# Kernel tuning notes

Measured on AMD Instinct MI355X. Metric: run time of the kernel, lower is better.

The kernel has to match this reference:

```python
import jax, jax.numpy as jnp
import numpy as np

N_HEAD = 16
HEAD_DIM = 64  # n_embd // n_head = 1024 // 16


def setup_inputs() -> dict:
    key = jax.random.key(0)
    k1, k2, k3 = jax.random.split(key, 3)
    B, T, C = 4, 2048, 1024
    x = jax.random.normal(k1, (B, T, C), dtype=jnp.float32)
    # torch Linear weight is (out, in); we store transposed (in, out) for x @ W
    w_qkv = jax.random.normal(k2, (C, 3 * C), dtype=jnp.float32) * (1.0 / np.sqrt(C))
    w_out = jax.random.normal(k3, (C, C), dtype=jnp.float32) * (1.0 / np.sqrt(C))
    return {"x": x, "w_qkv": w_qkv, "w_out": w_out}


def reference(x, w_qkv, w_out):
    B, T, C = x.shape
    scale = 1.0 / np.sqrt(HEAD_DIM).astype(np.float32)
    qkv = x @ w_qkv                                   # [B, T, 3C]
    q, k, v = jnp.split(qkv, 3, axis=2)
    def heads(t):  # [B, T, C] -> [B, H, T, Dh]
        return t.reshape(B, T, N_HEAD, HEAD_DIM).transpose(0, 2, 1, 3)
    q, k, v = heads(q), heads(k), heads(v)
    att = jnp.einsum('bhqd,bhkd->bhqk', q, k) * scale  # [B, H, T, T]
    causal = jnp.tril(jnp.ones((T, T), dtype=bool))
    att = jnp.where(causal[None, None], att, jnp.float32(-jnp.inf))
    att = jax.nn.softmax(att, axis=-1)
    y = jnp.einsum('bhqk,bhkd->bhqd', att, v)          # [B, H, T, Dh]
    y = y.transpose(0, 2, 1, 3).reshape(B, T, C)
    return y @ w_out
```

## Files before the change

kernel.cpp:

```cpp
#include <hip/hip_runtime.h>
#include <hip/hip_bf16.h>

#define B_ 4
#define T_ 2048
#define C_ 1024
#define H_ 16
#define D_ 64

typedef __bf16 bf16x8 __attribute__((ext_vector_type(8)));
typedef float f32x4 __attribute__((ext_vector_type(4)));
typedef float f32x16 __attribute__((ext_vector_type(16)));

__device__ __forceinline__ unsigned short f2bs(float f) {
    __hip_bfloat16 h = __float2bfloat16(f);
    return *reinterpret_cast<unsigned short*>(&h);
}

__device__ __forceinline__ float fexp2(float x) {
    float r;
    asm("v_exp_f32 %0, %1" : "=v"(r) : "v"(x));
    return r;
}

__device__ __forceinline__ unsigned cvtpk(float a, float b) {
    unsigned r;
    asm("v_cvt_pk_bf16_f32 %0, %1, %2" : "=v"(r) : "v"(a), "v"(b));
    return r;
}

__device__ __forceinline__ void plane32swap(unsigned& a, unsigned& b, int hi) {
#if __has_builtin(__builtin_amdgcn_permlane32_swap)
    typedef int i32x2 __attribute__((ext_vector_type(2)));
    i32x2 r = __builtin_amdgcn_permlane32_swap((int)a, (int)b, false, false);
    a = (unsigned)r.x; b = (unsigned)r.y;
#else
    unsigned v = hi ? a : b;
    unsigned e = __shfl_xor(v, 32);
    unsigned na = hi ? e : a;
    unsigned nb = hi ? b : e;
    a = na; b = nb;
#endif
}

__device__ __forceinline__ int swz(int row, int col) {
    return (row * 64 + col) ^ ((row & 7) << 3);
}

__device__ __forceinline__ void gload16(const void* g, void* l) {
    auto gp = (const __attribute__((address_space(1))) void*)(g);
    auto lp = (__attribute__((address_space(3))) void*)(uintptr_t)(l);
    __builtin_amdgcn_global_load_lds(gp, lp, 16, 0, 0);
}

__global__ __launch_bounds__(256)
void prep_fused(const float* __restrict__ x, unsigned short* __restrict__ xb,
                const float* __restrict__ in1, unsigned short* __restrict__ out1,
                const float* __restrict__ in2, unsigned short* __restrict__ out2) {
    __shared__ float tile[64][65];
    const int bid = blockIdx.x;
    if (bid < 8192) {
        int i = bid * 256 + threadIdx.x;
        float4 v = ((const float4*)x)[i];
        union { unsigned short h[4]; uint2 u; } pk;
        pk.h[0] = f2bs(v.x); pk.h[1] = f2bs(v.y);
        pk.h[2] = f2bs(v.z); pk.h[3] = f2bs(v.w);
        ((uint2*)xb)[i] = pk.u;
        return;
    }
    const int tb = bid - 8192;
    const int bx = tb & 63;
    const int by = tb >> 6;
    const int tx = threadIdx.x & 63;
    const int ty = threadIdx.x >> 6;
    const bool second = bx >= 48;
    const float* in = second ? in2 : in1;
    unsigned short* out = second ? out2 : out1;
    const int C = second ? 1024 : 3072;
    const int R = 1024;
    const int c0 = (second ? (bx - 48) : bx) * 64;
    const int r0 = by * 64;
    #pragma unroll
    for (int i = 0; i < 16; ++i) {
        int r = ty * 16 + i;
        tile[r][tx] = in[(size_t)(r0 + r) * C + c0 + tx];
    }
    __syncthreads();
    #pragma unroll
    for (int i = 0; i < 16; ++i) {
        int r = ty * 16 + i;
        out[(size_t)(c0 + r) * R + r0 + tx] = f2bs(tile[tx][r]);
    }
}

template<int MODE, int K>
__global__ __launch_bounds__(256, 5)
void gemm_bt32(const unsigned short* __restrict__ A,
               const unsigned short* __restrict__ Bt,
               float* __restrict__ Out, int N_out,
               unsigned short* __restrict__ Qb,
               unsigned short* __restrict__ Kb,
               unsigned short* __restrict__ Vt) {
    __shared__ alignas(16) unsigned short As[2][128 * 32];
    __shared__ alignas(16) unsigned short Bs[2][128 * 32];
    const int tid = threadIdx.x;
    const int l = tid & 63;
    const int c16 = l & 15, lq = l >> 4;
    const int wv = tid >> 6;
    const int wrow = wv >> 1, wcol = wv & 1;
    const int m0 = blockIdx.x * 128, n0 = blockIdx.y * 128;

    f32x4 acc[4][4];
    #pragma unroll
    for (int i = 0; i < 4; ++i)
        #pragma unroll
        for (int j = 0; j < 4; ++j)
            acc[i][j] = f32x4{0.f, 0.f, 0.f, 0.f};

    const int srow = tid >> 2;
    const int scs  = tid & 3;
    const int ldsbase = (tid & ~63) * 8;

    auto stage = [&](int k0, int buf) {
        #pragma unroll
        for (int p = 0; p < 2; ++p) {
            int row = p * 64 + srow;
            int csw = 8 * (scs ^ ((row >> 1) & 3));
            gload16(&A[(size_t)(m0 + row) * K + k0 + csw], &As[buf][p * 2048 + ldsbase]);
            gload16(&Bt[(size_t)(n0 + row) * K + k0 + csw], &Bs[buf][p * 2048 + ldsbase]);
        }
    };

    stage(0, 0);
    constexpr int NK = K >> 5;
    for (int i = 0; i < NK; ++i) {
        __syncthreads();
        if (i + 1 < NK) stage((i + 1) << 5, (i + 1) & 1);
        const unsigned short* Al = As[i & 1];
        const unsigned short* Bl = Bs[i & 1];
        bf16x8 af[4], bfv[4];
        #pragma unroll
        for (int t = 0; t < 4; ++t) {
            int arow = wrow * 64 + t * 16 + c16;
            int brow = wcol * 64 + t * 16 + c16;
            af[t]  = *(const bf16x8*)&Al[arow * 32 + ((lq ^ ((arow >> 1) & 3)) * 8)];
            bfv[t] = *(const bf16x8*)&Bl[brow * 32 + ((lq ^ ((brow >> 1) & 3)) * 8)];
        }
        #pragma unroll
        for (int mi = 0; mi < 4; ++mi)
            #pragma unroll
            for (int ni = 0; ni < 4; ++ni)
                acc[mi][ni] = __builtin_amdgcn_mfma_f32_16x16x32_bf16(
                    af[mi], bfv[ni], acc[mi][ni], 0, 0, 0);
    }

    #pragma unroll
    for (int mi = 0; mi < 4; ++mi) {
        #pragma unroll
        for (int ni = 0; ni < 4; ++ni) {
            #pragma unroll
            for (int r = 0; r < 4; ++r) {
                float v = acc[mi][ni][r];
                int row = m0 + wrow * 64 + mi * 16 + lq * 4 + r;
                int col = n0 + wcol * 64 + ni * 16 + c16;
                if (MODE == 1) {
                    Out[(size_t)row * N_out + col] = v;
                } else {
                    int which = col >> 10;
                    int c = col & 1023;
                    int h = c >> 6, d = c & 63;
                    int b = row >> 11, t = row & 2047;
                    int bh = b * H_ + h;
                    if (which == 0)
                        Qb[((size_t)(bh * T_ + t)) * D_ + d] = f2bs(v * 0.1803368801111204f);
                    else if (which == 1)
                        Kb[((size_t)(bh * T_ + t)) * D_ + d] = f2bs(v);
                    else
                        Vt[((size_t)(bh * D_ + d)) * T_ + t] = f2bs(v);
                }
            }
        }
    }
}

template<int MODE>
__global__ __launch_bounds__(256)
void gemm_bt(const unsigned short* __restrict__ A,
             const unsigned short* __restrict__ Bt,
             float* __restrict__ Out, int N_out,
             unsigned short* __restrict__ Qb,
             unsigned short* __restrict__ Kb,
             unsigned short* __restrict__ Vt,
             int K) {
    __shared__ alignas(16) unsigned short As[2][128 * 64];
    __shared__ alignas(16) unsigned short Bs[2][128 * 64];
    const int tid = threadIdx.x;
    const int l = tid & 63;
    const int c16 = l & 15, lq = l >> 4;
    const int wv = tid >> 6;
    const int wrow = wv >> 1, wcol = wv & 1;
    const int m0 = blockIdx.x * 128, n0 = blockIdx.y * 128;

    f32x4 acc[4][4];
    #pragma unroll
    for (int i = 0; i < 4; ++i)
        #pragma unroll
        for (int j = 0; j < 4; ++j)
            acc[i][j] = f32x4{0.f, 0.f, 0.f, 0.f};

    const int srow = tid >> 3;
    const int scs  = tid & 7;
    const int ldsbase = (tid & ~63) * 8;

    auto stage = [&](int k0, int buf) {
        #pragma unroll
        for (int p = 0; p < 4; ++p) {
            int row = p * 32 + srow;
            int csw = 8 * (scs ^ (row & 7));
            gload16(&A[(size_t)(m0 + row) * K + k0 + csw], &As[buf][p * 2048 + ldsbase]);
            gload16(&Bt[(size_t)(n0 + row) * K + k0 + csw], &Bs[buf][p * 2048 + ldsbase]);
        }
    };

    stage(0, 0);
    const int NK = K >> 6;
    for (int i = 0; i < NK; ++i) {
        __syncthreads();
        if (i + 1 < NK) stage((i + 1) << 6, (i + 1) & 1);
        const unsigned short* Al = As[i & 1];
        const unsigned short* Bl = Bs[i & 1];
        #pragma unroll
        for (int kk = 0; kk < 64; kk += 32) {
            bf16x8 af[4], bfv[4];
            int koff = kk + lq * 8;
            #pragma unroll
            for (int t = 0; t < 4; ++t) {
                af[t]  = *(const bf16x8*)&Al[swz(wrow * 64 + t * 16 + c16, koff)];
                bfv[t] = *(const bf16x8*)&Bl[swz(wcol * 64 + t * 16 + c16, koff)];
            }
            #pragma unroll
            for (int mi = 0; mi < 4; ++mi)
                #pragma unroll
                for (int ni = 0; ni < 4; ++ni)
                    acc[mi][ni] = __builtin_amdgcn_mfma_f32_16x16x32_bf16(
                        af[mi], bfv[ni], acc[mi][ni], 0, 0, 0);
        }
    }

    #pragma unroll
    for (int mi = 0; mi < 4; ++mi) {
        #pragma unroll
        for (int ni = 0; ni < 4; ++ni) {
            #pragma unroll
            for (int r = 0; r < 4; ++r) {
                float v = acc[mi][ni][r];
                int row = m0 + wrow * 64 + mi * 16 + lq * 4 + r;
                int col = n0 + wcol * 64 + ni * 16 + c16;
                if (MODE == 1) {
                    Out[(size_t)row * N_out + col] = v;
                } else {
                    int which = col >> 10;
                    int c = col & 1023;
                    int h = c >> 6, d = c & 63;
                    int b = row >> 11, t = row & 2047;
                    int bh = b * H_ + h;
                    if (which == 0)
                        Qb[((size_t)(bh * T_ + t)) * D_ + d] = f2bs(v * 0.1803368801111204f);
                    else if (which == 1)
                        Kb[((size_t)(bh * T_ + t)) * D_ + d] = f2bs(v);
                    else
                        Vt[((size_t)(bh * D_ + d)) * T_ + t] = f2bs(v);
                }
            }
        }
    }
}

__global__ __launch_bounds__(256, 2)
void attn_fwd(const unsigned short* __restrict__ Qb,
              const unsigned short* __restrict__ Kb,
              const unsigned short* __restrict__ Vt,
              unsigned short* __restrict__ Y) {
    __shared__ alignas(16) unsigned short Ks[2][64 * 64];
    __shared__ alignas(16) unsigned short Vs[2][64 * 64];
    const int tid = threadIdx.x;
    const int wv = tid >> 6;
    const int l = tid & 63;
    const int r32 = l & 31;
    const int hi = l >> 5;
    const int hi8 = hi * 8;
    const int bh = blockIdx.x & 63;
    const int qp = blockIdx.x >> 6;
    const unsigned short* Kp = Kb + (size_t)bh * T_ * D_;
    const unsigned short* Vp = Vt + (size_t)bh * D_ * T_;
    const unsigned short* Qbase = Qb + (size_t)bh * T_ * D_;
    const int b = bh >> 4, h = bh & 15;
    const int srow = tid >> 3;
    const int scs  = tid & 7;
    const int scol_sw = 8 * (scs ^ (srow & 7));
    const int wbase = wv * 512;

    #pragma unroll
    for (int half = 0; half < 2; ++half) {
        const int qc = (half == 0) ? qp : 15 - qp;
        const int q0w = qc * 128 + wv * 32;
        const int nt = 2 * qc + 2;
        const int qg = q0w + r32;

        bf16x8 qf[4];
        #pragma unroll
        for (int ds = 0; ds < 4; ++ds)
            qf[ds] = *(const bf16x8*)&Qbase[(size_t)qg * 64 + ds * 16 + hi8];

        f32x16 o[2];
        #pragma unroll
        for (int e = 0; e < 16; ++e) { o[0][e] = 0.f; o[1][e] = 0.f; }
        float lsum = 0.f;

        __syncthreads();
        gload16(&Kp[(size_t)srow * 64 + scol_sw],        &Ks[0][wbase]);
        gload16(&Kp[(size_t)(srow + 32) * 64 + scol_sw], &Ks[0][2048 + wbase]);
        gload16(&Vp[(size_t)srow * T_ + scol_sw],        &Vs[0][wbase]);
        gload16(&Vp[(size_t)(srow + 32) * T_ + scol_sw], &Vs[0][2048 + wbase]);

        for (int it = 0; it < nt; ++it) {
            const int kb = it * 64;
            __syncthreads();
            if (it + 1 < nt) {
                const int kn = kb + 64;
                unsigned short* Kd = Ks[(it + 1) & 1];
                unsigned short* Vd = Vs[(it + 1) & 1];
                gload16(&Kp[(size_t)(kn + srow) * 64 + scol_sw],        &Kd[wbase]);
                gload16(&Kp[(size_t)(kn + srow + 32) * 64 + scol_sw],   &Kd[2048 + wbase]);
                gload16(&Vp[(size_t)srow * T_ + kn + scol_sw],          &Vd[wbase]);
                gload16(&Vp[(size_t)(srow + 32) * T_ + kn + scol_sw],   &Vd[2048 + wbase]);
            }
            if (kb > q0w + 31) continue;
            const unsigned short* Kl = Ks[it & 1];
            const unsigned short* Vl = Vs[it & 1];

            f32x16 s[2];
            #pragma unroll
            for (int e = 0; e < 16; ++e) { s[0][e] = 0.f; s[1][e] = 0.f; }
            __builtin_amdgcn_s_setprio(1);
            #pragma unroll
            for (int kt = 0; kt < 2; ++kt)
                #pragma unroll
                for (int ds = 0; ds < 4; ++ds) {
                    bf16x8 af = *(const bf16x8*)&Kl[swz(32 * kt + r32, ds * 16 + hi8)];
                    s[kt] = __builtin_amdgcn_mfma_f32_32x32x16_bf16(af, qf[ds], s[kt], 0, 0, 0);
                }
            __builtin_amdgcn_s_setprio(0);
            if (kb + 63 > q0w) {
                #pragma unroll
                for (int kt = 0; kt < 2; ++kt)
                    #pragma unroll
                    for (int m = 0; m < 4; ++m)
                        #pragma unroll
                        for (int r = 0; r < 4; ++r)
                            if (kb + 32 * kt + 8 * m + r + 4 * hi > qg)
                                s[kt][4 * m + r] = -1e30f;
            }
            float rs0 = 0.f, rs1 = 0.f, rs2 = 0.f, rs3 = 0.f;
            #pragma unroll
            for (int kt = 0; kt < 2; ++kt)
                #pragma unroll
                for (int m = 0; m < 4; ++m) {
                    float p0 = fexp2(s[kt][4 * m + 0]);
                    float p1 = fexp2(s[kt][4 * m + 1]);
                    float p2 = fexp2(s[kt][4 * m + 2]);
                    float p3 = fexp2(s[kt][4 * m + 3]);
                    s[kt][4 * m + 0] = p0; s[kt][4 * m + 1] = p1;
                    s[kt][4 * m + 2] = p2; s[kt][4 * m + 3] = p3;
                    rs0 += p0; rs1 += p1; rs2 += p2; rs3 += p3;
                }
            lsum += (rs0 + rs1) + (rs2 + rs3);
            bf16x8 pb[4];
            #pragma unroll
            for (int ks = 0; ks < 4; ++ks) {
                const int kt = ks >> 1;
                const int m0 = (ks & 1) * 2;
                unsigned a0 = cvtpk(s[kt][4 * m0 + 0], s[kt][4 * m0 + 1]);
                unsigned a1 = cvtpk(s[kt][4 * m0 + 2], s[kt][4 * m0 + 3]);
                unsigned b0 = cvtpk(s[kt][4 * m0 + 4], s[kt][4 * m0 + 5]);
                unsigned b1 = cvtpk(s[kt][4 * m0 + 6], s[kt][4 * m0 + 7]);
                plane32swap(a0, b0, hi);
                plane32swap(a1, b1, hi);
                uint4 u = {a0, a1, b0, b1};
                pb[ks] = *reinterpret_cast<bf16x8*>(&u);
            }
            __builtin_amdgcn_s_setprio(1);
            #pragma unroll
            for (int dt = 0; dt < 2; ++dt)
                #pragma unroll
                for (int ks = 0; ks < 4; ++ks) {
                    bf16x8 va = *(const bf16x8*)&Vl[swz(32 * dt + r32, ks * 16 + hi8)];
                    o[dt] = __builtin_amdgcn_mfma_f32_32x32x16_bf16(va, pb[ks], o[dt], 0, 0, 0);
                }
            __builtin_amdgcn_s_setprio(0);
        }

        float lt = lsum + __shfl_xor(lsum, 32);
        float inv = 1.f / lt;
        #pragma unroll
        for (int dt = 0; dt < 2; ++dt)
            #pragma unroll
            for (int m = 0; m < 4; ++m) {
                uint2 w;
                w.x = cvtpk(o[dt][4 * m + 0] * inv, o[dt][4 * m + 1] * inv);
                w.y = cvtpk(o[dt][4 * m + 2] * inv, o[dt][4 * m + 3] * inv);
                int d = 32 * dt + 8 * m + 4 * hi;
                *(uint2*)&Y[((size_t)(b * T_ + qg)) * C_ + h * D_ + d] = w;
            }
    }
}

extern "C" void kernel_launch(void* const* d_in, const int* in_sizes, int n_in,
                              void* d_out, int out_size, void* d_ws, size_t ws_size,
                              hipStream_t stream) {
    const float* x     = (const float*)d_in[0];
    const float* w_qkv = (const float*)d_in[1];
    const float* w_out = (const float*)d_in[2];
    float* out = (float*)d_out;
    char* ws = (char*)d_ws;

    unsigned short* xb  = (unsigned short*)(ws);
    unsigned short* wqt = (unsigned short*)(ws + (16u << 20));
    unsigned short* wot = (unsigned short*)(ws + (22u << 20));
    unsigned short* Qb  = (unsigned short*)(ws + (24u << 20));
    unsigned short* Kb  = (unsigned short*)(ws + (40u << 20));
    unsigned short* Vt  = (unsigned short*)(ws + (56u << 20));
    unsigned short* Yb  = (unsigned short*)(ws + (72u << 20));

    prep_fused<<<9216, 256, 0, stream>>>(x, xb, w_qkv, wqt, w_out, wot);
    gemm_bt32<0, 1024><<<dim3(64, 24), 256, 0, stream>>>(xb, wqt, nullptr, 3072, Qb, Kb, Vt);
    attn_fwd<<<512, 256, 0, stream>>>(Qb, Kb, Vt, Yb);
    gemm_bt<1><<<dim3(64, 8), 256, 0, stream>>>(Yb, wot, out, 1024, nullptr, nullptr, nullptr, 1024);
}
```

Before: 171.2 us.

## Triple-buffer QKV GEMM with BK=64 and split attention into one chunk per block

The QKV projection GEMM moves from double-buffered 32-wide K tiles to triple-buffered 64-wide K tiles. It uses explicit vmcnt waits and raw barriers so that loads two stages ahead overlap the MFMA work. The attention kernel drops its paired balanced-halves loop and launches 1024 blocks with one query chunk each, heaviest chunks first, with occupancy raised to 4 blocks per CU. This trades the explicit load balancing for more parallelism and relies on block scheduling order, and the larger LDS footprint may lower GEMM occupancy.

```diff
diff --git a/kernel.cpp b/kernel.cpp
--- a/kernel.cpp
+++ b/kernel.cpp
@@ -93,15 +93,15 @@
 }
 
 template<int MODE, int K>
-__global__ __launch_bounds__(256, 5)
-void gemm_bt32(const unsigned short* __restrict__ A,
-               const unsigned short* __restrict__ Bt,
-               float* __restrict__ Out, int N_out,
-               unsigned short* __restrict__ Qb,
-               unsigned short* __restrict__ Kb,
-               unsigned short* __restrict__ Vt) {
-    __shared__ alignas(16) unsigned short As[2][128 * 32];
-    __shared__ alignas(16) unsigned short Bs[2][128 * 32];
+__global__ __launch_bounds__(256)
+void gemm_bt3(const unsigned short* __restrict__ A,
+              const unsigned short* __restrict__ Bt,
+              float* __restrict__ Out, int N_out,
+              unsigned short* __restrict__ Qb,
+              unsigned short* __restrict__ Kb,
+              unsigned short* __restrict__ Vt) {
+    __shared__ alignas(16) unsigned short As[3][128 * 64];
+    __shared__ alignas(16) unsigned short Bs[3][128 * 64];
     const int tid = threadIdx.x;
     const int l = tid & 63;
     const int c16 = l & 15, lq = l >> 4;
@@ -116,41 +116,53 @@
         for (int j = 0; j < 4; ++j)
             acc[i][j] = f32x4{0.f, 0.f, 0.f, 0.f};
 
-    const int srow = tid >> 2;
-    const int scs  = tid & 3;
+    const int srow = tid >> 3;
+    const int scs  = tid & 7;
     const int ldsbase = (tid & ~63) * 8;
 
-    auto stage = [&](int k0, int buf) {
-        #pragma unroll
-        for (int p = 0; p < 2; ++p) {
-            int row = p * 64 + srow;
-            int csw = 8 * (scs ^ ((row >> 1) & 3));
-            gload16(&A[(size_t)(m0 + row) * K + k0 + csw], &As[buf][p * 2048 + ldsbase]);
-            gload16(&Bt[(size_t)(n0 + row) * K + k0 + csw], &Bs[buf][p * 2048 + ldsbase]);
+    auto stage = [&](int k0, int b) {
+        #pragma unroll
+        for (int p = 0; p < 4; ++p) {
+            int row = p * 32 + srow;
+            int csw = 8 * (scs ^ (row & 7));
+            gload16(&A[(size_t)(m0 + row) * K + k0 + csw], &As[b][p * 2048 + ldsbase]);
+            gload16(&Bt[(size_t)(n0 + row) * K + k0 + csw], &Bs[b][p * 2048 + ldsbase]);
         }
     };
 
     stage(0, 0);
-    constexpr int NK = K >> 5;
+    if (K > 64) stage(64, 1);
+    constexpr int NK = K >> 6;
+    int cur = 0;
     for (int i = 0; i < NK; ++i) {
-        __syncthreads();
-        if (i + 1 < NK) stage((i + 1) << 5, (i + 1) & 1);
-        const unsigned short* Al = As[i & 1];
-        const unsigned short* Bl = Bs[i & 1];
-        bf16x8 af[4], bfv[4];
-        #pragma unroll
-        for (int t = 0; t < 4; ++t) {
-            int arow = wrow * 64 + t * 16 + c16;
-            int brow = wcol * 64 + t * 16 + c16;
-            af[t]  = *(const bf16x8*)&Al[arow * 32 + ((lq ^ ((arow >> 1) & 3)) * 8)];
-            bfv[t] = *(const bf16x8*)&Bl[brow * 32 + ((lq ^ ((brow >> 1) & 3)) * 8)];
-        }
-        #pragma unroll
-        for (int mi = 0; mi < 4; ++mi)
-            #pragma unroll
-            for (int ni = 0; ni < 4; ++ni)
-                acc[mi][ni] = __builtin_amdgcn_mfma_f32_16x16x32_bf16(
-                    af[mi], bfv[ni], acc[mi][ni], 0, 0, 0);
+        __builtin_amdgcn_sched_barrier(0x7);
+        if (i == NK - 1) asm volatile("s_waitcnt vmcnt(0)" ::: "memory");
+        else             asm volatile("s_waitcnt vmcnt(8)" ::: "memory");
+        __builtin_amdgcn_s_barrier();
+        __builtin_amdgcn_sched_barrier(0x7);
+        if (i + 2 < NK) {
+            int nb = cur + 2; if (nb >= 3) nb -= 3;
+            stage((i + 2) << 6, nb);
+        }
+        const unsigned short* Al = As[cur];
+        const unsigned short* Bl = Bs[cur];
+        #pragma unroll
+        for (int kk = 0; kk < 64; kk += 32) {
+            bf16x8 af[4], bfv[4];
+            int koff = kk + lq * 8;
+            #pragma unroll
+            for (int t = 0; t < 4; ++t) {
+                af[t]  = *(const bf16x8*)&Al[swz(wrow * 64 + t * 16 + c16, koff)];
+                bfv[t] = *(const bf16x8*)&Bl[swz(wcol * 64 + t * 16 + c16, koff)];
+            }
+            #pragma unroll
+            for (int mi = 0; mi < 4; ++mi)
+                #pragma unroll
+                for (int ni = 0; ni < 4; ++ni)
+                    acc[mi][ni] = __builtin_amdgcn_mfma_f32_16x16x32_bf16(
+                        af[mi], bfv[ni], acc[mi][ni], 0, 0, 0);
+        }
+        ++cur; if (cur >= 3) cur -= 3;
     }
 
     #pragma unroll
@@ -275,7 +287,7 @@
     }
 }
 
-__global__ __launch_bounds__(256, 2)
+__global__ __launch_bounds__(256, 4)
 void attn_fwd(const unsigned short* __restrict__ Qb,
               const unsigned short* __restrict__ Kb,
               const unsigned short* __restrict__ Vt,
@@ -289,7 +301,7 @@
     const int hi = l >> 5;
     const int hi8 = hi * 8;
     const int bh = blockIdx.x & 63;
-    const int qp = blockIdx.x >> 6;
+    const int qc = 15 - (blockIdx.x >> 6);
     const unsigned short* Kp = Kb + (size_t)bh * T_ * D_;
     const unsigned short* Vp = Vt + (size_t)bh * D_ * T_;
     const unsigned short* Qbase = Qb + (size_t)bh * T_ * D_;
@@ -299,119 +311,114 @@
     const int scol_sw = 8 * (scs ^ (srow & 7));
     const int wbase = wv * 512;
 
-    #pragma unroll
-    for (int half = 0; half < 2; ++half) {
-        const int qc = (half == 0) ? qp : 15 - qp;
-        const int q0w = qc * 128 + wv * 32;
-        const int nt = 2 * qc + 2;
-        const int qg = q0w + r32;
-
-        bf16x8 qf[4];
-        #pragma unroll
-        for (int ds = 0; ds < 4; ++ds)
-            qf[ds] = *(const bf16x8*)&Qbase[(size_t)qg * 64 + ds * 16 + hi8];
-
-        f32x16 o[2];
-        #pragma unroll
-        for (int e = 0; e < 16; ++e) { o[0][e] = 0.f; o[1][e] = 0.f; }
-        float lsum = 0.f;
-
+    const int q0w = qc * 128 + wv * 32;
+    const int nt = 2 * qc + 2;
+    const int qg = q0w + r32;
+
+    bf16x8 qf[4];
+    #pragma unroll
+    for (int ds = 0; ds < 4; ++ds)
+        qf[ds] = *(const bf16x8*)&Qbase[(size_t)qg * 64 + ds * 16 + hi8];
+
+    f32x16 o[2];
+    #pragma unroll
+    for (int e = 0; e < 16; ++e) { o[0][e] = 0.f; o[1][e] = 0.f; }
+    float lsum = 0.f;
+
+    gload16(&Kp[(size_t)srow * 64 + scol_sw],        &Ks[0][wbase]);
+    gload16(&Kp[(size_t)(srow + 32) * 64 + scol_sw], &Ks[0][2048 + wbase]);
+    gload16(&Vp[(size_t)srow * T_ + scol_sw],        &Vs[0][wbase]);
+    gload16(&Vp[(size_t)(srow + 32) * T_ + scol_sw], &Vs[0][2048 + wbase]);
+
+    for (int it = 0; it < nt; ++it) {
+        const int kb = it * 64;
         __syncthreads();
-        gload16(&Kp[(size_t)srow * 64 + scol_sw],        &Ks[0][wbase]);
-        gload16(&Kp[(size_t)(srow + 32) * 64 + scol_sw], &Ks[0][2048 + wbase]);
-        gload16(&Vp[(size_t)srow * T_ + scol_sw],        &Vs[0][wbase]);
-        gload16(&Vp[(size_t)(srow + 32) * T_ + scol_sw], &Vs[0][2048 + wbase]);
-
-        for (int it = 0; it < nt; ++it) {
-            const int kb = it * 64;
-            __syncthreads();
-            if (it + 1 < nt) {
-                const int kn = kb + 64;
-                unsigned short* Kd = Ks[(it + 1) & 1];
-                unsigned short* Vd = Vs[(it + 1) & 1];
-                gload16(&Kp[(size_t)(kn + srow) * 64 + scol_sw],        &Kd[wbase]);
-                gload16(&Kp[(size_t)(kn + srow + 32) * 64 + scol_sw],   &Kd[2048 + wbase]);
-                gload16(&Vp[(size_t)srow * T_ + kn + scol_sw],          &Vd[wbase]);
-                gload16(&Vp[(size_t)(srow + 32) * T_ + kn + scol_sw],   &Vd[2048 + wbase]);
-            }
-            if (kb > q0w + 31) continue;
-            const unsigned short* Kl = Ks[it & 1];
-            const unsigned short* Vl = Vs[it & 1];
-
-            f32x16 s[2];
-            #pragma unroll
-            for (int e = 0; e < 16; ++e) { s[0][e] = 0.f; s[1][e] = 0.f; }
-            __builtin_amdgcn_s_setprio(1);
+        if (it + 1 < nt) {
+            const int kn = kb + 64;
+            unsigned short* Kd = Ks[(it + 1) & 1];
+            unsigned short* Vd = Vs[(it + 1) & 1];
+            gload16(&Kp[(size_t)(kn + srow) * 64 + scol_sw],        &Kd[wbase]);
+            gload16(&Kp[(size_t)(kn + srow + 32) * 64 + scol_sw],   &Kd[2048 + wbase]);
+            gload16(&Vp[(size_t)srow * T_ + kn + scol_sw],          &Vd[wbase]);
+            gload16(&Vp[(size_t)(srow + 32) * T_ + kn + scol_sw],   &Vd[2048 + wbase]);
+        }
+        if (kb > q0w + 31) continue;
+        const unsigned short* Kl = Ks[it & 1];
+        const unsigned short* Vl = Vs[it & 1];
+
+        f32x16 s[2];
+        #pragma unroll
+        for (int e = 0; e < 16; ++e) { s[0][e] = 0.f; s[1][e] = 0.f; }
+        __builtin_amdgcn_s_setprio(1);
+        #pragma unroll
+        for (int kt = 0; kt < 2; ++kt)
+            #pragma unroll
+            for (int ds = 0; ds < 4; ++ds) {
+                bf16x8 af = *(const bf16x8*)&Kl[swz(32 * kt + r32, ds * 16 + hi8)];
+                s[kt] = __builtin_amdgcn_mfma_f32_32x32x16_bf16(af, qf[ds], s[kt], 0, 0, 0);
+            }
+        __builtin_amdgcn_s_setprio(0);
+        if (kb + 63 > q0w) {
             #pragma unroll
             for (int kt = 0; kt < 2; ++kt)
                 #pragma unroll
-                for (int ds = 0; ds < 4; ++ds) {
-                    bf16x8 af = *(const bf16x8*)&Kl[swz(32 * kt + r32, ds * 16 + hi8)];
-                    s[kt] = __builtin_amdgcn_mfma_f32_32x32x16_bf16(af, qf[ds], s[kt], 0, 0, 0);
-                }
-            __builtin_amdgcn_s_setprio(0);
-            if (kb + 63 > q0w) {
-                #pragma unroll
-                for (int kt = 0; kt < 2; ++kt)
+                for (int m = 0; m < 4; ++m)
                     #pragma unroll
-                    for (int m = 0; m < 4; ++m)
-                        #pragma unroll
-                        for (int r = 0; r < 4; ++r)
-                            if (kb + 32 * kt + 8 * m + r + 4 * hi > qg)
-                                s[kt][4 * m + r] = -1e30f;
-            }
-            float rs0 = 0.f, rs1 = 0.f, rs2 = 0.f, rs3 = 0.f;
-            #pragma unroll
-            for (int kt = 0; kt < 2; ++kt)
-                #pragma unroll
-                for (int m = 0; m < 4; ++m) {
-                    float p0 = fexp2(s[kt][4 * m + 0]);
-                    float p1 = fexp2(s[kt][4 * m + 1]);
-                    float p2 = fexp2(s[kt][4 * m + 2]);
-                    float p3 = fexp2(s[kt][4 * m + 3]);
-                    s[kt][4 * m + 0] = p0; s[kt][4 * m + 1] = p1;
-                    s[kt][4 * m + 2] = p2; s[kt][4 * m + 3] = p3;
-                    rs0 += p0; rs1 += p1; rs2 += p2; rs3 += p3;
-                }
-            lsum += (rs0 + rs1) + (rs2 + rs3);
-            bf16x8 pb[4];
+                    for (int r = 0; r < 4; ++r)
+                        if (kb + 32 * kt + 8 * m + r + 4 * hi > qg)
+                            s[kt][4 * m + r] = -1e30f;
+        }
+        float rs0 = 0.f, rs1 = 0.f, rs2 = 0.f, rs3 = 0.f;
+        #pragma unroll
+        for (int kt = 0; kt < 2; ++kt)
+            #pragma unroll
+            for (int m = 0; m < 4; ++m) {
+                float p0 = fexp2(s[kt][4 * m + 0]);
+                float p1 = fexp2(s[kt][4 * m + 1]);
+                float p2 = fexp2(s[kt][4 * m + 2]);
+                float p3 = fexp2(s[kt][4 * m + 3]);
+                s[kt][4 * m + 0] = p0; s[kt][4 * m + 1] = p1;
+                s[kt][4 * m + 2] = p2; s[kt][4 * m + 3] = p3;
+                rs0 += p0; rs1 += p1; rs2 += p2; rs3 += p3;
+            }
+        lsum += (rs0 + rs1) + (rs2 + rs3);
+        bf16x8 pb[4];
+        #pragma unroll
+        for (int ks = 0; ks < 4; ++ks) {
+            const int kt = ks >> 1;
+            const int m0 = (ks & 1) * 2;
+            unsigned a0 = cvtpk(s[kt][4 * m0 + 0], s[kt][4 * m0 + 1]);
+            unsigned a1 = cvtpk(s[kt][4 * m0 + 2], s[kt][4 * m0 + 3]);
+            unsigned b0 = cvtpk(s[kt][4 * m0 + 4], s[kt][4 * m0 + 5]);
+            unsigned b1 = cvtpk(s[kt][4 * m0 + 6], s[kt][4 * m0 + 7]);
+            plane32swap(a0, b0, hi);
+            plane32swap(a1, b1, hi);
+            uint4 u = {a0, a1, b0, b1};
+            pb[ks] = *reinterpret_cast<bf16x8*>(&u);
+        }
+        __builtin_amdgcn_s_setprio(1);
+        #pragma unroll
+        for (int dt = 0; dt < 2; ++dt)
             #pragma unroll
             for (int ks = 0; ks < 4; ++ks) {
-                const int kt = ks >> 1;
-                const int m0 = (ks & 1) * 2;
-                unsigned a0 = cvtpk(s[kt][4 * m0 + 0], s[kt][4 * m0 + 1]);
-                unsigned a1 = cvtpk(s[kt][4 * m0 + 2], s[kt][4 * m0 + 3]);
-                unsigned b0 = cvtpk(s[kt][4 * m0 + 4], s[kt][4 * m0 + 5]);
-                unsigned b1 = cvtpk(s[kt][4 * m0 + 6], s[kt][4 * m0 + 7]);
-                plane32swap(a0, b0, hi);
-                plane32swap(a1, b1, hi);
-                uint4 u = {a0, a1, b0, b1};
-                pb[ks] = *reinterpret_cast<bf16x8*>(&u);
-            }
-            __builtin_amdgcn_s_setprio(1);
-            #pragma unroll
-            for (int dt = 0; dt < 2; ++dt)
-                #pragma unroll
-                for (int ks = 0; ks < 4; ++ks) {
-                    bf16x8 va = *(const bf16x8*)&Vl[swz(32 * dt + r32, ks * 16 + hi8)];
-                    o[dt] = __builtin_amdgcn_mfma_f32_32x32x16_bf16(va, pb[ks], o[dt], 0, 0, 0);
-                }
-            __builtin_amdgcn_s_setprio(0);
-        }
-
-        float lt = lsum + __shfl_xor(lsum, 32);
-        float inv = 1.f / lt;
-        #pragma unroll
-        for (int dt = 0; dt < 2; ++dt)
-            #pragma unroll
-            for (int m = 0; m < 4; ++m) {
-                uint2 w;
-                w.x = cvtpk(o[dt][4 * m + 0] * inv, o[dt][4 * m + 1] * inv);
-                w.y = cvtpk(o[dt][4 * m + 2] * inv, o[dt][4 * m + 3] * inv);
-                int d = 32 * dt + 8 * m + 4 * hi;
-                *(uint2*)&Y[((size_t)(b * T_ + qg)) * C_ + h * D_ + d] = w;
-            }
-    }
+                bf16x8 va = *(const bf16x8*)&Vl[swz(32 * dt + r32, ks * 16 + hi8)];
+                o[dt] = __builtin_amdgcn_mfma_f32_32x32x16_bf16(va, pb[ks], o[dt], 0, 0, 0);
+            }
+        __builtin_amdgcn_s_setprio(0);
+    }
+
+    float lt = lsum + __shfl_xor(lsum, 32);
+    float inv = 1.f / lt;
+    #pragma unroll
+    for (int dt = 0; dt < 2; ++dt)
+        #pragma unroll
+        for (int m = 0; m < 4; ++m) {
+            uint2 w;
+            w.x = cvtpk(o[dt][4 * m + 0] * inv, o[dt][4 * m + 1] * inv);
+            w.y = cvtpk(o[dt][4 * m + 2] * inv, o[dt][4 * m + 3] * inv);
+            int d = 32 * dt + 8 * m + 4 * hi;
+            *(uint2*)&Y[((size_t)(b * T_ + qg)) * C_ + h * D_ + d] = w;
+        }
 }
 
 extern "C" void kernel_launch(void* const* d_in, const int* in_sizes, int n_in,
@@ -432,7 +439,7 @@
     unsigned short* Yb  = (unsigned short*)(ws + (72u << 20));
 
     prep_fused<<<9216, 256, 0, stream>>>(x, xb, w_qkv, wqt, w_out, wot);
-    gemm_bt32<0, 1024><<<dim3(64, 24), 256, 0, stream>>>(xb, wqt, nullptr, 3072, Qb, Kb, Vt);
-    attn_fwd<<<512, 256, 0, stream>>>(Qb, Kb, Vt, Yb);
+    gemm_bt3<0, 1024><<<dim3(64, 24), 256, 0, stream>>>(xb, wqt, nullptr, 3072, Qb, Kb, Vt);
+    attn_fwd<<<1024, 256, 0, stream>>>(Qb, Kb, Vt, Yb);
     gemm_bt<1><<<dim3(64, 8), 256, 0, stream>>>(Yb, wot, out, 1024, nullptr, nullptr, nullptr, 1024);
 }
```

Result: slower. 189.5 us (+10.7%).
